# Optimization experiments

Hardware: AMD Instinct MI355X
Metric: run time of the kernel (lower is better)

## Reference

```python
import jax, jax.numpy as jnp
import numpy as np

N, DIM, RF_DIM, H, W, PN, TOPK = 16, 2048, 256, 16, 8, 64, 10  # TOPK = 2*k = 2*(K//2)


def conv1x1(w, x):
    # w: [O, C] (1x1 conv kernel), x: [b, C, h, w] -> [b, O, h, w]
    return jnp.einsum('oc,bchw->bohw', w, x)


def calibration(x, y):
    # x, y: [b, c, h, w]
    b, c, h, w = x.shape
    xv = x.reshape(b, c, h * w)
    yv = y.reshape(b, c, h * w)
    c_aff = jax.nn.softmax(jnp.einsum('bcm,bdm->bcd', xv, yv), axis=2)  # [b,c,c]
    s_aff = jax.nn.softmax(jnp.einsum('bcm,bcn->bmn', xv, yv), axis=2)  # [b,hw,hw]
    c_avg = c_aff.mean(axis=-1)  # [b,c]
    s_avg = s_aff.mean(axis=-1)  # [b,hw]
    aff = (c_avg[:, :, None] * s_avg[:, None, :]).reshape(b, c, h, w)
    pos = jax.nn.relu(aff - 0.5) + 0.5
    comp = jax.nn.relu(0.5 - aff) + 0.5
    return x * pos + y * comp


def instance_norm(x, eps=1e-5):
    m = x.mean(axis=(2, 3), keepdims=True)
    v = x.var(axis=(2, 3), keepdims=True)
    return (x - m) * jax.lax.rsqrt(v + eps)


def setup_inputs():
    key = jax.random.key(0)
    ks = jax.random.split(key, 6)
    return {
        'inputs': jax.random.normal(ks[0], (N, DIM, H, W), jnp.float32),
        'mv_prototype': jax.random.normal(ks[1], (PN, DIM, H, W), jnp.float32),
        'w_rf': jax.random.normal(ks[2], (RF_DIM, DIM), jnp.float32) * 0.02,
        'w_rf_mv': jax.random.normal(ks[3], (DIM, TOPK * RF_DIM), jnp.float32) * 0.02,
        'w_rm_s': jax.random.normal(ks[4], (DIM, DIM), jnp.float32) * 0.02,
        'w_fuse': jax.random.normal(ks[5], (DIM, DIM), jnp.float32) * 0.02,
    }


def reference(inputs, mv_prototype, w_rf, w_rf_mv, w_rm_s, w_fuse):
    n, c, h, w = inputs.shape
    # pairwise squared euclidean distance (addmm-style cdist)
    xf = inputs.reshape(n, -1)
    pf = mv_prototype.reshape(mv_prototype.shape[0], -1)
    dist = (xf * xf).sum(1, keepdims=True) + (pf * pf).sum(1)[None, :] - 2.0 * xf @ pf.T
    idx = jnp.argsort(dist, axis=1)[:, :TOPK]  # [n, 2k] nearest prototypes
    # refine prototypes then gather per-sample top-2k and stack channels
    xp = conv1x1(w_rf, mv_prototype)  # [pn, rf_dim, h, w]
    mv_list = xp[idx].reshape(n, TOPK * RF_DIM, h, w)
    mvl = conv1x1(w_rf_mv, mv_list)  # [n, dim, h, w]
    mvl = jax.nn.relu(calibration(inputs, mvl))
    mv_a = instance_norm(conv1x1(w_rm_s, mvl))
    x_fuse = jax.nn.sigmoid(conv1x1(w_fuse, mv_a))
    return inputs + inputs * x_fuse
```

## Files before the change

### kernel.cpp

```cpp
#include <hip/hip_runtime.h>
#include <cstdint>
#include <cstddef>

#define N_    16
#define DIM_  2048
#define RF_   256
#define PN_   64
#define TOPK_ 10
#define HW_   128
#define KFULL (DIM_*HW_)
#define KMV   (TOPK_*RF_)

#define AS1 __attribute__((address_space(1)))
#define AS3 __attribute__((address_space(3)))

typedef __attribute__((ext_vector_type(8))) short bf16x8;
typedef __attribute__((ext_vector_type(4))) float f32x4;
typedef __attribute__((ext_vector_type(8))) unsigned short u16x8;

__device__ __forceinline__ unsigned short f2bf(float f) {
  unsigned u = __builtin_bit_cast(unsigned, f);
  unsigned r = (u + 0x7FFFu + ((u >> 16) & 1u)) >> 16;
  return (unsigned short)r;
}

template <int O, int C>
__device__ __forceinline__ void cvt_tensor(const float* __restrict__ s,
                                           unsigned short* __restrict__ d,
                                           int gid, int stride) {
  const int G = O * (C / 8);
  for (int j = gid; j < G; j += stride) {
    int o = j / (C / 8);
    int cg = j - o * (C / 8);
    const float4 a = *(const float4*)(s + (size_t)o * C + (size_t)cg * 8);
    const float4 b = *(const float4*)(s + (size_t)o * C + (size_t)cg * 8 + 4);
    u16x8 pk;
    pk[0] = f2bf(a.x); pk[1] = f2bf(a.y); pk[2] = f2bf(a.z); pk[3] = f2bf(a.w);
    pk[4] = f2bf(b.x); pk[5] = f2bf(b.y); pk[6] = f2bf(b.z); pk[7] = f2bf(b.w);
    *(u16x8*)(d + (size_t)cg * (O * 8) + (size_t)o * 8) = pk;
  }
}

__global__ __launch_bounds__(256)
void cvt_all_kernel(const float* __restrict__ s0, const float* __restrict__ s1,
                    const float* __restrict__ s2, const float* __restrict__ s3,
                    unsigned short* __restrict__ d0, unsigned short* __restrict__ d1,
                    unsigned short* __restrict__ d2, unsigned short* __restrict__ d3,
                    float* __restrict__ dsum) {
  int gid = blockIdx.x * blockDim.x + threadIdx.x;
  if (gid < 1152) dsum[gid] = 0.f;
  int stride = gridDim.x * blockDim.x;
  cvt_tensor<RF_,  DIM_>(s0, d0, gid, stride);
  cvt_tensor<DIM_, KMV >(s1, d1, gid, stride);
  cvt_tensor<DIM_, DIM_>(s2, d2, gid, stride);
  cvt_tensor<DIM_, DIM_>(s3, d3, gid, stride);
}

__global__ __launch_bounds__(256)
void transpose_proto_kernel(const float* __restrict__ src, unsigned short* __restrict__ dst) {
  __shared__ float tile[32][129];
  const int p = blockIdx.x;
  const int c0 = blockIdx.y * 32;
  const int t = threadIdx.x;
  const float* sp = src + ((size_t)p * DIM_ + c0) * HW_;
#pragma unroll
  for (int i = 0; i < 4; ++i) {
    int g = i * 256 + t;
    int ci = g >> 5, s4 = g & 31;
    float4 v = *(const float4*)(sp + (size_t)ci * HW_ + s4 * 4);
    int sb = s4 * 4;
    tile[ci][sb] = v.x; tile[ci][sb + 1] = v.y; tile[ci][sb + 2] = v.z; tile[ci][sb + 3] = v.w;
  }
  __syncthreads();
  unsigned short* dp = dst + (size_t)p * HW_ * DIM_ + (size_t)(c0 >> 3) * 1024;
#pragma unroll
  for (int i = 0; i < 2; ++i) {
    int cidx = i * 256 + t;
    int kg = cidx >> 7, s = cidx & 127;
    u16x8 pk;
#pragma unroll
    for (int u = 0; u < 8; ++u) pk[u] = f2bf(tile[kg * 8 + u][s]);
    *(u16x8*)(dp + (size_t)kg * 1024 + (size_t)s * 8) = pk;
  }
}

__global__ __launch_bounds__(256)
void dist_partial_kernel(const float* __restrict__ x, const float* __restrict__ proto,
                         float* __restrict__ dsum) {
  __shared__ alignas(16) float xl[16][132];
  __shared__ alignas(16) float pl[64][132];
  const int t = threadIdx.x, b = blockIdx.x;
  const int n0 = t & 7;
  const int pb = t >> 3;
  float acc[2][2] = {};
  float pn = 0.f;

  for (int sc = 0; sc < 4; ++sc) {
    const int k0 = b * 512 + sc * 128;
#pragma unroll
    for (int it = 0; it < 2; ++it) {
      int f = it * 256 + t;
      int row = f >> 5, s4 = f & 31;
      *(float4*)&xl[row][s4 * 4] = *(const float4*)(x + (size_t)row * KFULL + k0 + s4 * 4);
    }
#pragma unroll
    for (int it = 0; it < 8; ++it) {
      int f = it * 256 + t;
      int row = f >> 5, s4 = f & 31;
      *(float4*)&pl[row][s4 * 4] = *(const float4*)(proto + (size_t)row * KFULL + k0 + s4 * 4);
    }
    __syncthreads();

#pragma unroll 4
    for (int k = 0; k < 128; k += 4) {
      float4 xa = *(float4*)&xl[n0][k];
      float4 xb = *(float4*)&xl[n0 + 8][k];
      float4 p0 = *(float4*)&pl[pb][k];
      float4 p1 = *(float4*)&pl[pb + 32][k];
      acc[0][0] += xa.x*p0.x + xa.y*p0.y + xa.z*p0.z + xa.w*p0.w;
      acc[0][1] += xa.x*p1.x + xa.y*p1.y + xa.z*p1.z + xa.w*p1.w;
      acc[1][0] += xb.x*p0.x + xb.y*p0.y + xb.z*p0.z + xb.w*p0.w;
      acc[1][1] += xb.x*p1.x + xb.y*p1.y + xb.z*p1.z + xb.w*p1.w;
    }
    if (t < 64) {
#pragma unroll 4
      for (int k = 0; k < 128; k += 4) {
        float4 pv = *(float4*)&pl[t][k];
        pn += pv.x*pv.x + pv.y*pv.y + pv.z*pv.z + pv.w*pv.w;
      }
    }
    __syncthreads();
  }

  atomicAdd(&dsum[n0 * 64 + pb],        -2.f * acc[0][0]);
  atomicAdd(&dsum[n0 * 64 + pb + 32],   -2.f * acc[0][1]);
  atomicAdd(&dsum[(n0+8) * 64 + pb],    -2.f * acc[1][0]);
  atomicAdd(&dsum[(n0+8) * 64 + pb+32], -2.f * acc[1][1]);
  if (t < 64) atomicAdd(&dsum[1024 + t], pn);
}

__global__ __launch_bounds__(64)
void select_kernel(const float* __restrict__ dsum, int* __restrict__ idx,
                   int* __restrict__ flags) {
  __shared__ float sh[64];
  const int n = blockIdx.x, t = threadIdx.x;
  float dval = dsum[1024 + t] + dsum[n * 64 + t];
  sh[t] = dval;
  __syncthreads();
  int rank = 0;
#pragma unroll
  for (int j = 0; j < 64; ++j) {
    float o = sh[j];
    rank += (o < dval || (o == dval && j < t)) ? 1 : 0;
  }
  if (rank < TOPK_) { idx[n * TOPK_ + rank] = t; flags[t] = 1; }
}

#define BM 64
#define BKK 64

template <int MODE>
__global__ __launch_bounds__(128, 2)
void mfma_gemm_kernel(const unsigned short* __restrict__ Wb,
                      const unsigned short* __restrict__ Xb,
                      void* __restrict__ OutP,
                      const float* __restrict__ inputs,
                      const int* __restrict__ idxp,
                      const int* __restrict__ flags,
                      int K, int O, int Ldim) {
  __shared__ alignas(16) unsigned short Al[3][8 * BM * 8];
  __shared__ alignas(16) unsigned short Bl[3][8 * 128 * 8];

  const int t = threadIdx.x;
  const int w = t >> 6;
  const int lane = t & 63;
  const int q = lane >> 4;
  const int l15 = lane & 15;
  const int batch = blockIdx.y;
  const int o0 = blockIdx.x * BM;

  if (MODE == 0 && flags && !flags[batch]) return;

  int idreg = 0;
  if (MODE == 1 && lane < TOPK_) idreg = idxp[batch * TOPK_ + lane];

  f32x4 acc[4][4] = {};

  auto issue = [&](int k0, int buf) {
#pragma unroll
    for (int i = 0; i < 4; ++i) {
      int qk = w * 4 + i;
      const unsigned short* ga =
          Wb + (size_t)((k0 >> 3) + qk) * (O * 8) + (size_t)(o0 + lane) * 8;
      __builtin_amdgcn_global_load_lds((const AS1 void*)ga,
                                       (AS3 void*)(&Al[buf][qk * 512]), 16, 0, 0);
    }
    const unsigned short* base;
    if (MODE == 1) {
      int id = __shfl(idreg, k0 >> 8, 64);
      base = Xb + (size_t)id * (HW_ * RF_) + (size_t)((k0 & 255) >> 3) * 1024;
    } else {
      base = Xb + (size_t)batch * HW_ * K + (size_t)(k0 >> 3) * 1024;
    }
#pragma unroll
    for (int i = 0; i < 8; ++i) {
      int v = w * 8 + i;
      int qk = v >> 1, h = v & 1;
      const unsigned short* gb = base + (size_t)qk * 1024 + (size_t)(h * 64 + lane) * 8;
      __builtin_amdgcn_global_load_lds((const AS1 void*)gb,
                                       (AS3 void*)(&Bl[buf][qk * 1024 + h * 512]), 16, 0, 0);
    }
  };

  const int nIter = K / BKK;

  issue(0, 0);
  issue(BKK, 1);

  for (int it = 0; it < nIter; ++it) {
    const int buf = it % 3;
    if (it + 1 < nIter) {
      asm volatile("s_waitcnt vmcnt(12)" ::: "memory");
    } else {
      asm volatile("s_waitcnt vmcnt(0)" ::: "memory");
    }
    __builtin_amdgcn_s_barrier();
#pragma unroll
    for (int s = 0; s < 2; ++s) {
      bf16x8 af[4], bfr[4];
#pragma unroll
      for (int mt = 0; mt < 4; ++mt)
        af[mt] = *(const bf16x8*)(&Al[buf][(s * 4 + q) * 512 + (mt * 16 + l15) * 8]);
#pragma unroll
      for (int nt = 0; nt < 4; ++nt)
        bfr[nt] = *(const bf16x8*)(&Bl[buf][(s * 4 + q) * 1024 + (w * 64 + nt * 16 + l15) * 8]);
#pragma unroll
      for (int mt = 0; mt < 4; ++mt)
#pragma unroll
        for (int nt = 0; nt < 4; ++nt)
          acc[mt][nt] = __builtin_amdgcn_mfma_f32_16x16x32_bf16(af[mt], bfr[nt], acc[mt][nt], 0, 0, 0);
    }
    if (it + 2 < nIter) issue((it + 2) * BKK, (it + 2) % 3);
  }

  const float CAL = 1.0f - 1.0f / 262144.0f;

  float* nsumS = (float*)&Al[0][0];
  float* nsqS  = (float*)&Al[0][0] + 128;

  if (MODE == 2) {
#pragma unroll
    for (int mt = 0; mt < 4; ++mt)
#pragma unroll
      for (int reg = 0; reg < 4; ++reg) {
        float s_ = 0.f, q_ = 0.f;
#pragma unroll
        for (int nt = 0; nt < 4; ++nt) {
          float v = acc[mt][nt][reg];
          s_ += v; q_ += v * v;
        }
#pragma unroll
        for (int m = 1; m < 16; m <<= 1) {
          s_ += __shfl_xor(s_, m, 64);
          q_ += __shfl_xor(q_, m, 64);
        }
        if (l15 == 0) {
          int ol = mt * 16 + q * 4 + reg;
          nsumS[w * 64 + ol] = s_; nsqS[w * 64 + ol] = q_;
        }
      }
    __syncthreads();
  }

  if (MODE == 3) {
    float* ofb = (float*)OutP + (size_t)batch * DIM_ * HW_;
    const float* inb = inputs + (size_t)batch * DIM_ * HW_;
#pragma unroll
    for (int mt = 0; mt < 4; ++mt)
#pragma unroll
      for (int nt = 0; nt < 4; ++nt) {
        int o = o0 + mt * 16 + q * 4;
        int s = w * 64 + nt * 16 + l15;
        f32x4 v = acc[mt][nt];
#pragma unroll
        for (int g = 0; g < 4; ++g) {
          float in = inb[(size_t)(o + g) * HW_ + s];
          float sg = 1.f / (1.f + expf(-v[g]));
          ofb[(size_t)(o + g) * HW_ + s] = in * (1.f + sg);
        }
      }
  } else {
    unsigned short* ob = (unsigned short*)OutP + (size_t)batch * HW_ * Ldim;
    const float* inb = (MODE == 1) ? inputs + (size_t)batch * DIM_ * HW_ : nullptr;
#pragma unroll
    for (int mt = 0; mt < 4; ++mt) {
      float mean[4], rs[4];
      if (MODE == 2) {
#pragma unroll
        for (int reg = 0; reg < 4; ++reg) {
          int ol = mt * 16 + q * 4 + reg;
          float ts = nsumS[ol] + nsumS[64 + ol];
          float tq = nsqS[ol] + nsqS[64 + ol];
          float mn = ts * (1.f / 128.f);
          float vr = tq * (1.f / 128.f) - mn * mn;
          mean[reg] = mn; rs[reg] = rsqrtf(vr + 1e-5f);
        }
      }
#pragma unroll
      for (int nt = 0; nt < 4; ++nt) {
        int o = o0 + mt * 16 + q * 4;
        int s = w * 64 + nt * 16 + l15;
        f32x4 v = acc[mt][nt];
        float r[4];
        if (MODE == 0) {
#pragma unroll
          for (int g = 0; g < 4; ++g) r[g] = v[g];
        } else if (MODE == 1) {
          const float* ip = inb + (size_t)o * HW_ + s;
#pragma unroll
          for (int g = 0; g < 4; ++g)
            r[g] = fmaxf(0.f, 0.5f * ip[(size_t)g * HW_] + CAL * v[g]);
        } else {
#pragma unroll
          for (int g = 0; g < 4; ++g) r[g] = (v[g] - mean[g]) * rs[g];
        }
        ushort4 pk;
        pk.x = f2bf(r[0]); pk.y = f2bf(r[1]); pk.z = f2bf(r[2]); pk.w = f2bf(r[3]);
        *(ushort4*)(ob + (size_t)(o >> 3) * 1024 + (size_t)s * 8 + (o & 7)) = pk;
      }
    }
  }
}

extern "C" void kernel_launch(void* const* d_in, const int* in_sizes, int n_in,
                              void* d_out, int out_size, void* d_ws, size_t ws_size,
                              hipStream_t stream) {
  const float* inputs = (const float*)d_in[0];
  const float* proto  = (const float*)d_in[1];
  const float* w_rf   = (const float*)d_in[2];
  const float* w_rfmv = (const float*)d_in[3];
  const float* w_rms  = (const float*)d_in[4];
  const float* w_fuse = (const float*)d_in[5];
  float* out = (float*)d_out;

  uint8_t* ws = (uint8_t*)d_ws;
  size_t off = 0;
  auto alloc = [&](size_t bytes) { uint8_t* p = ws + off; off += (bytes + 255) & ~(size_t)255; return p; };

  float* dsum  = (float*)alloc(1088 * 4);
  int*   flags = (int*)alloc(PN_ * 4);
  int*   idx   = (int*)alloc(N_ * TOPK_ * 4);
  unsigned short* wrf_b   = (unsigned short*)alloc((size_t)RF_ * DIM_ * 2);
  unsigned short* wrfmv_b = (unsigned short*)alloc((size_t)DIM_ * KMV * 2);
  unsigned short* wrms_b  = (unsigned short*)alloc((size_t)DIM_ * DIM_ * 2);
  unsigned short* wfuse_b = (unsigned short*)alloc((size_t)DIM_ * DIM_ * 2);
  unsigned short* xpT     = (unsigned short*)alloc((size_t)PN_ * HW_ * RF_ * 2);
  unsigned short* protoT  = (unsigned short*)alloc((size_t)PN_ * HW_ * DIM_ * 2);
  unsigned short* mvlT = protoT;
  unsigned short* mvaT = protoT + (size_t)N_ * HW_ * DIM_;

  cvt_all_kernel<<<1024, 256, 0, stream>>>(w_rf, w_rfmv, w_rms, w_fuse,
                                           wrf_b, wrfmv_b, wrms_b, wfuse_b, dsum);
  transpose_proto_kernel<<<dim3(PN_, DIM_ / 32), 256, 0, stream>>>(proto, protoT);
  dist_partial_kernel<<<512, 256, 0, stream>>>(inputs, proto, dsum);
  select_kernel<<<N_, 64, 0, stream>>>(dsum, idx, flags);

  mfma_gemm_kernel<0><<<dim3(RF_ / BM, PN_), 128, 0, stream>>>(
      wrf_b, protoT, xpT, nullptr, nullptr, flags, DIM_, RF_, RF_);
  mfma_gemm_kernel<1><<<dim3(DIM_ / BM, N_), 128, 0, stream>>>(
      wrfmv_b, xpT, mvlT, inputs, idx, nullptr, KMV, DIM_, DIM_);
  mfma_gemm_kernel<2><<<dim3(DIM_ / BM, N_), 128, 0, stream>>>(
      wrms_b, mvlT, mvaT, nullptr, nullptr, nullptr, DIM_, DIM_, DIM_);
  mfma_gemm_kernel<3><<<dim3(DIM_ / BM, N_), 128, 0, stream>>>(
      wfuse_b, mvaT, out, inputs, nullptr, nullptr, DIM_, DIM_, DIM_);
}
```

Measured before the change: 376.5 us.

## Tile weight conversion through LDS, move proto norms into transpose, double-buffer distance

The weight-to-bf16 conversion now stages 64x32 tiles in shared memory, so the transposed stores are written in contiguous runs instead of strided scatters. Prototype squared norms are computed in the transpose kernel with a wave reduction and an atomic, which removes the extra norm loop from the distance kernel. The distance kernel switches to 64-wide chunks with register-staged double buffering so global loads overlap the dot-product loop. The trade-offs are more shared memory use, more atomics, and a grid size that is hard-coded to the tile counts.

Result: slower. 444.0 us (+17.9%).

```diff
diff --git a/kernel.cpp b/kernel.cpp
--- a/kernel.cpp
+++ b/kernel.cpp
@@ -24,53 +24,70 @@
   return (unsigned short)r;
 }
 
-template <int O, int C>
-__device__ __forceinline__ void cvt_tensor(const float* __restrict__ s,
-                                           unsigned short* __restrict__ d,
-                                           int gid, int stride) {
-  const int G = O * (C / 8);
-  for (int j = gid; j < G; j += stride) {
-    int o = j / (C / 8);
-    int cg = j - o * (C / 8);
-    const float4 a = *(const float4*)(s + (size_t)o * C + (size_t)cg * 8);
-    const float4 b = *(const float4*)(s + (size_t)o * C + (size_t)cg * 8 + 4);
-    u16x8 pk;
-    pk[0] = f2bf(a.x); pk[1] = f2bf(a.y); pk[2] = f2bf(a.z); pk[3] = f2bf(a.w);
-    pk[4] = f2bf(b.x); pk[5] = f2bf(b.y); pk[6] = f2bf(b.z); pk[7] = f2bf(b.w);
-    *(u16x8*)(d + (size_t)cg * (O * 8) + (size_t)o * 8) = pk;
-  }
-}
-
 __global__ __launch_bounds__(256)
 void cvt_all_kernel(const float* __restrict__ s0, const float* __restrict__ s1,
                     const float* __restrict__ s2, const float* __restrict__ s3,
                     unsigned short* __restrict__ d0, unsigned short* __restrict__ d1,
                     unsigned short* __restrict__ d2, unsigned short* __restrict__ d3,
                     float* __restrict__ dsum) {
-  int gid = blockIdx.x * blockDim.x + threadIdx.x;
+  __shared__ u16x8 tile[32][65];
+  const int t = threadIdx.x;
+  int gid = blockIdx.x * 256 + t;
   if (gid < 1152) dsum[gid] = 0.f;
-  int stride = gridDim.x * blockDim.x;
-  cvt_tensor<RF_,  DIM_>(s0, d0, gid, stride);
-  cvt_tensor<DIM_, KMV >(s1, d1, gid, stride);
-  cvt_tensor<DIM_, DIM_>(s2, d2, gid, stride);
-  cvt_tensor<DIM_, DIM_>(s3, d3, gid, stride);
+
+  int bid = blockIdx.x;
+  const float* s; unsigned short* d; int O, CG, tb;
+  if (bid < 32)       { s = s0; d = d0; O = RF_;  CG = DIM_ / 8; tb = bid; }
+  else if (bid < 352) { s = s1; d = d1; O = DIM_; CG = KMV  / 8; tb = bid - 32; }
+  else if (bid < 608) { s = s2; d = d2; O = DIM_; CG = DIM_ / 8; tb = bid - 352; }
+  else                { s = s3; d = d3; O = DIM_; CG = DIM_ / 8; tb = bid - 608; }
+  const int nCgT = CG / 32;
+  const int o0  = (tb / nCgT) * 64;
+  const int cg0 = (tb % nCgT) * 32;
+  const size_t C = (size_t)CG * 8;
+
+#pragma unroll
+  for (int i = 0; i < 8; ++i) {
+    int idx = i * 256 + t, ol = idx >> 5, cg = idx & 31;
+    const float* sp = s + (size_t)(o0 + ol) * C + (size_t)(cg0 + cg) * 8;
+    float4 a = *(const float4*)sp;
+    float4 b = *(const float4*)(sp + 4);
+    u16x8 pk;
+    pk[0] = f2bf(a.x); pk[1] = f2bf(a.y); pk[2] = f2bf(a.z); pk[3] = f2bf(a.w);
+    pk[4] = f2bf(b.x); pk[5] = f2bf(b.y); pk[6] = f2bf(b.z); pk[7] = f2bf(b.w);
+    tile[cg][ol] = pk;
+  }
+  __syncthreads();
+#pragma unroll
+  for (int i = 0; i < 8; ++i) {
+    int idx = i * 256 + t, cg = idx >> 6, ol = idx & 63;
+    *(u16x8*)(d + (size_t)(cg0 + cg) * ((size_t)O * 8) + (size_t)(o0 + ol) * 8) =
+        tile[cg][ol];
+  }
 }
 
 __global__ __launch_bounds__(256)
-void transpose_proto_kernel(const float* __restrict__ src, unsigned short* __restrict__ dst) {
+void transpose_proto_kernel(const float* __restrict__ src,
+                            unsigned short* __restrict__ dst,
+                            float* __restrict__ dsum) {
   __shared__ float tile[32][129];
   const int p = blockIdx.x;
   const int c0 = blockIdx.y * 32;
   const int t = threadIdx.x;
   const float* sp = src + ((size_t)p * DIM_ + c0) * HW_;
+  float sq = 0.f;
 #pragma unroll
   for (int i = 0; i < 4; ++i) {
     int g = i * 256 + t;
     int ci = g >> 5, s4 = g & 31;
     float4 v = *(const float4*)(sp + (size_t)ci * HW_ + s4 * 4);
+    sq += v.x * v.x + v.y * v.y + v.z * v.z + v.w * v.w;
     int sb = s4 * 4;
     tile[ci][sb] = v.x; tile[ci][sb + 1] = v.y; tile[ci][sb + 2] = v.z; tile[ci][sb + 3] = v.w;
   }
+#pragma unroll
+  for (int m = 1; m < 64; m <<= 1) sq += __shfl_xor(sq, m, 64);
+  if ((t & 63) == 0) atomicAdd(&dsum[1024 + p], sq);
   __syncthreads();
   unsigned short* dp = dst + (size_t)p * HW_ * DIM_ + (size_t)(c0 >> 3) * 1024;
 #pragma unroll
@@ -87,56 +104,57 @@
 __global__ __launch_bounds__(256)
 void dist_partial_kernel(const float* __restrict__ x, const float* __restrict__ proto,
                          float* __restrict__ dsum) {
-  __shared__ alignas(16) float xl[16][132];
-  __shared__ alignas(16) float pl[64][132];
+  __shared__ alignas(16) float xl[2][16][68];
+  __shared__ alignas(16) float pl[2][64][68];
   const int t = threadIdx.x, b = blockIdx.x;
-  const int n0 = t & 7;
-  const int pb = t >> 3;
+  const int n0 = t & 7, pb = t >> 3;
+  const int xr = t >> 4, xc = (t & 15) * 4;
   float acc[2][2] = {};
-  float pn = 0.f;
-
-  for (int sc = 0; sc < 4; ++sc) {
-    const int k0 = b * 512 + sc * 128;
-#pragma unroll
-    for (int it = 0; it < 2; ++it) {
-      int f = it * 256 + t;
-      int row = f >> 5, s4 = f & 31;
-      *(float4*)&xl[row][s4 * 4] = *(const float4*)(x + (size_t)row * KFULL + k0 + s4 * 4);
-    }
-#pragma unroll
-    for (int it = 0; it < 8; ++it) {
-      int f = it * 256 + t;
-      int row = f >> 5, s4 = f & 31;
-      *(float4*)&pl[row][s4 * 4] = *(const float4*)(proto + (size_t)row * KFULL + k0 + s4 * 4);
-    }
-    __syncthreads();
-
-#pragma unroll 4
-    for (int k = 0; k < 128; k += 4) {
-      float4 xa = *(float4*)&xl[n0][k];
-      float4 xb = *(float4*)&xl[n0 + 8][k];
-      float4 p0 = *(float4*)&pl[pb][k];
-      float4 p1 = *(float4*)&pl[pb + 32][k];
+  const size_t kbase = (size_t)b * 512;
+
+  float4 rx, rp[4];
+  auto gload = [&](int ph) {
+    const size_t k0 = kbase + ph * 64;
+    rx = *(const float4*)(x + (size_t)xr * KFULL + k0 + xc);
+#pragma unroll
+    for (int i = 0; i < 4; ++i) {
+      int idx = i * 256 + t;
+      rp[i] = *(const float4*)(proto + (size_t)(idx >> 4) * KFULL + k0 + (idx & 15) * 4);
+    }
+  };
+  auto swrite = [&](int buf) {
+    *(float4*)&xl[buf][xr][xc] = rx;
+#pragma unroll
+    for (int i = 0; i < 4; ++i) {
+      int idx = i * 256 + t;
+      *(float4*)&pl[buf][idx >> 4][(idx & 15) * 4] = rp[i];
+    }
+  };
+
+  gload(0); swrite(0);
+  __syncthreads();
+  for (int ph = 0; ph < 8; ++ph) {
+    const int buf = ph & 1;
+    if (ph + 1 < 8) gload(ph + 1);
+#pragma unroll 8
+    for (int k = 0; k < 64; k += 4) {
+      float4 xa = *(float4*)&xl[buf][n0][k];
+      float4 xb = *(float4*)&xl[buf][n0 + 8][k];
+      float4 p0 = *(float4*)&pl[buf][pb][k];
+      float4 p1 = *(float4*)&pl[buf][pb + 32][k];
       acc[0][0] += xa.x*p0.x + xa.y*p0.y + xa.z*p0.z + xa.w*p0.w;
       acc[0][1] += xa.x*p1.x + xa.y*p1.y + xa.z*p1.z + xa.w*p1.w;
       acc[1][0] += xb.x*p0.x + xb.y*p0.y + xb.z*p0.z + xb.w*p0.w;
       acc[1][1] += xb.x*p1.x + xb.y*p1.y + xb.z*p1.z + xb.w*p1.w;
     }
-    if (t < 64) {
-#pragma unroll 4
-      for (int k = 0; k < 128; k += 4) {
-        float4 pv = *(float4*)&pl[t][k];
-        pn += pv.x*pv.x + pv.y*pv.y + pv.z*pv.z + pv.w*pv.w;
-      }
-    }
+    if (ph + 1 < 8) swrite(buf ^ 1);
     __syncthreads();
   }
 
-  atomicAdd(&dsum[n0 * 64 + pb],        -2.f * acc[0][0]);
-  atomicAdd(&dsum[n0 * 64 + pb + 32],   -2.f * acc[0][1]);
-  atomicAdd(&dsum[(n0+8) * 64 + pb],    -2.f * acc[1][0]);
-  atomicAdd(&dsum[(n0+8) * 64 + pb+32], -2.f * acc[1][1]);
-  if (t < 64) atomicAdd(&dsum[1024 + t], pn);
+  atomicAdd(&dsum[n0 * 64 + pb],          -2.f * acc[0][0]);
+  atomicAdd(&dsum[n0 * 64 + pb + 32],     -2.f * acc[0][1]);
+  atomicAdd(&dsum[(n0 + 8) * 64 + pb],    -2.f * acc[1][0]);
+  atomicAdd(&dsum[(n0 + 8) * 64 + pb + 32], -2.f * acc[1][1]);
 }
 
 __global__ __launch_bounds__(64)
@@ -359,9 +377,9 @@
   unsigned short* mvlT = protoT;
   unsigned short* mvaT = protoT + (size_t)N_ * HW_ * DIM_;
 
-  cvt_all_kernel<<<1024, 256, 0, stream>>>(w_rf, w_rfmv, w_rms, w_fuse,
-                                           wrf_b, wrfmv_b, wrms_b, wfuse_b, dsum);
-  transpose_proto_kernel<<<dim3(PN_, DIM_ / 32), 256, 0, stream>>>(proto, protoT);
+  cvt_all_kernel<<<864, 256, 0, stream>>>(w_rf, w_rfmv, w_rms, w_fuse,
+                                          wrf_b, wrfmv_b, wrms_b, wfuse_b, dsum);
+  transpose_proto_kernel<<<dim3(PN_, DIM_ / 32), 256, 0, stream>>>(proto, protoT, dsum);
   dist_partial_kernel<<<512, 256, 0, stream>>>(inputs, proto, dsum);
   select_kernel<<<N_, 64, 0, stream>>>(dsum, idx, flags);
 
```
